# Performance work log

Hardware: AMD Instinct MI355X
Metric: run time of the kernel (lower is better)

Reference implementation:

```python
import jax, jax.numpy as jnp
import numpy as np

EPS_NORM = 1e-8
EPS_Q = 1e-5

def rmsnorm(x, g):
    var = jnp.mean(x * x, axis=-1, keepdims=True)
    return x * jax.lax.rsqrt(var + EPS_NORM) * g

def activation_quant(x):
    # per-token int8 absmax quantization
    scale = 127.0 / jnp.clip(jnp.max(jnp.abs(x), axis=-1, keepdims=True), EPS_Q, None)
    return jnp.clip(jnp.round(x * scale), -128.0, 127.0) / scale

def weight_quant(w):
    # per-tensor ternary absmean quantization
    scale = 1.0 / jnp.clip(jnp.mean(jnp.abs(w)), EPS_Q, None)
    return jnp.clip(jnp.round(w * scale), -1.0, 1.0) / scale

def ste(x, qfn):
    # straight-through estimator: forward quantized, backward identity
    return x + jax.lax.stop_gradient(qfn(x) - x)

def bitlinear(x, w, g):
    h = rmsnorm(x, g)
    hq = ste(h, activation_quant)
    wq = ste(w, weight_quant)
    return jnp.einsum('bsh,oh->bso', hq, wq)

def setup_inputs() -> dict:
    key = jax.random.key(0)
    k1, k2, k3 = jax.random.split(key, 3)
    B, S, H = 2, 2048, 2048
    I = int(H * 4.0)  # intermediate_size = 8192
    x = jax.random.normal(k1, (B, S, H), dtype=jnp.float32)
    w_gate = jax.random.normal(k2, (2 * I, H), dtype=jnp.float32) * 0.02
    g_gate = jnp.ones((H,), dtype=jnp.float32)
    w_down = jax.random.normal(k3, (H, I), dtype=jnp.float32) * 0.02
    g_down = jnp.ones((I,), dtype=jnp.float32)
    return {"x": x, "w_gate": w_gate, "g_gate": g_gate, "w_down": w_down, "g_down": g_down}

def reference(x, w_gate, g_gate, w_down, g_down):
    y = bitlinear(x, w_gate, g_gate)        # [B,S,2I]
    gate, up = jnp.split(y, 2, axis=-1)     # each [B,S,I]
    z = bitlinear(jax.nn.silu(gate) * up, w_down, g_down)  # [B,S,H]
    return z
```

## Files before the change

kernel.cpp:

```cpp
#include <hip/hip_runtime.h>
#include <hip/hip_bf16.h>
#include <hip/hip_fp16.h>

#define DEVINL __device__ __forceinline__

typedef float f32x4 __attribute__((ext_vector_type(4)));
typedef int i32x4 __attribute__((ext_vector_type(4)));
typedef unsigned int u32x4 __attribute__((ext_vector_type(4)));
typedef unsigned int u32x2 __attribute__((ext_vector_type(2)));

typedef __attribute__((address_space(1))) void void_g;
typedef __attribute__((address_space(3))) void void_l;

DEVINL void gload16(const void* g, void* l) {
  __builtin_amdgcn_global_load_lds((void_g*)g, (void_l*)l, 16, 0, 0);
}

DEVINL float wave_sum(float v) {
  #pragma unroll
  for (int o = 32; o > 0; o >>= 1) v += __shfl_down(v, o, 64);
  return v;
}
DEVINL float wave_max(float v) {
  #pragma unroll
  for (int o = 32; o > 0; o >>= 1) v = fmaxf(v, __shfl_down(v, o, 64));
  return v;
}

DEVINL unsigned int pack4(float a, float b, float c, float d) {
  return ((unsigned int)(unsigned char)(signed char)(int)a)
       | (((unsigned int)(unsigned char)(signed char)(int)b) << 8)
       | (((unsigned int)(unsigned char)(signed char)(int)c) << 16)
       | (((unsigned int)(unsigned char)(signed char)(int)d) << 24);
}

__global__ __launch_bounds__(256) void absum_kernel(const float* __restrict__ w,
                                                    long long nchunk, double* __restrict__ out) {
  long long stride = (long long)gridDim.x * 256;
  long long i = (long long)blockIdx.x * 256 + threadIdx.x;
  float s = 0.f;
  for (; i < nchunk; i += stride) {
    f32x4 v = ((const f32x4*)w)[i];
    s += fabsf(v[0]) + fabsf(v[1]) + fabsf(v[2]) + fabsf(v[3]);
  }
  s = wave_sum(s);
  __shared__ float red[4];
  int lane = threadIdx.x & 63, wv = threadIdx.x >> 6;
  if (lane == 0) red[wv] = s;
  __syncthreads();
  if (threadIdx.x == 0) atomicAdd(out, (double)(red[0] + red[1] + red[2] + red[3]));
}

__global__ __launch_bounds__(256) void quantw_kernel(const float* __restrict__ w,
                                                     signed char* __restrict__ tern,
                                                     long long nchunk,
                                                     const double* __restrict__ sum, double inv_n) {
  float scale = (float)(1.0 / fmax(*sum * inv_n, 1e-5));
  long long stride = (long long)gridDim.x * 256;
  long long i = (long long)blockIdx.x * 256 + threadIdx.x;
  for (; i < nchunk; i += stride) {
    f32x4 v0 = ((const f32x4*)w)[2 * i];
    f32x4 v1 = ((const f32x4*)w)[2 * i + 1];
    float t[8];
    #pragma unroll
    for (int k = 0; k < 4; k++) {
      t[k]     = fminf(fmaxf(rintf(v0[k] * scale), -1.f), 1.f);
      t[4 + k] = fminf(fmaxf(rintf(v1[k] * scale), -1.f), 1.f);
    }
    u32x2 o;
    o[0] = pack4(t[0], t[1], t[2], t[3]);
    o[1] = pack4(t[4], t[5], t[6], t[7]);
    ((u32x2*)tern)[i] = o;
  }
}

__global__ __launch_bounds__(256) void actq1_kernel(const float* __restrict__ x,
                                                    const float* __restrict__ g,
                                                    signed char* __restrict__ q,
                                                    float* __restrict__ a) {
  int t = blockIdx.x, tid = threadIdx.x;
  int lane = tid & 63, wv = tid >> 6;
  __shared__ float redS[4], redM[4];

  const f32x4* xr = (const f32x4*)(x + (size_t)t * 2048);
  f32x4 v0 = xr[tid * 2], v1 = xr[tid * 2 + 1];
  float ssq = 0.f;
  #pragma unroll
  for (int k = 0; k < 4; k++) ssq += v0[k] * v0[k] + v1[k] * v1[k];
  float ws_ = wave_sum(ssq);
  if (lane == 0) redS[wv] = ws_;
  __syncthreads();
  float tot = redS[0] + redS[1] + redS[2] + redS[3];
  float r = rsqrtf(tot / 2048.f + 1e-8f);

  f32x4 g0 = ((const f32x4*)g)[tid * 2], g1 = ((const f32x4*)g)[tid * 2 + 1];
  float h[8], amax = 0.f;
  #pragma unroll
  for (int k = 0; k < 4; k++) {
    h[k]     = v0[k] * r * g0[k];
    h[4 + k] = v1[k] * r * g1[k];
    amax = fmaxf(amax, fmaxf(fabsf(h[k]), fabsf(h[4 + k])));
  }
  float wm = wave_max(amax);
  if (lane == 0) redM[wv] = wm;
  __syncthreads();
  float am = fmaxf(fmaxf(fmaxf(redM[0], redM[1]), fmaxf(redM[2], redM[3])), 1e-5f);
  float scale = 127.f / am;

  float qv[8];
  #pragma unroll
  for (int k = 0; k < 8; k++) qv[k] = fminf(fmaxf(rintf(h[k] * scale), -128.f), 127.f);
  u32x2 o;
  o[0] = pack4(qv[0], qv[1], qv[2], qv[3]);
  o[1] = pack4(qv[4], qv[5], qv[6], qv[7]);
  ((u32x2*)(q + (size_t)t * 2048))[tid] = o;
  if (tid == 0) a[t] = am / 127.f;
}

__global__ __launch_bounds__(256) void silu_rms_q_kernel(const unsigned short* __restrict__ y,
                                                         const float* __restrict__ g,
                                                         signed char* __restrict__ q2,
                                                         float* __restrict__ a2) {
  int t = blockIdx.x, tid = threadIdx.x;
  int lane = tid & 63, wv = tid >> 6;
  __shared__ float redS[4], redM[4];
  const u32x4* gate = (const u32x4*)(y + (size_t)t * 16384);
  const u32x4* up   = (const u32x4*)(y + (size_t)t * 16384 + 8192);

  float v[32];
  float ssq = 0.f;
  #pragma unroll
  for (int b = 0; b < 4; b++) {
    u32x4 gr = gate[b * 256 + tid];
    u32x4 ur = up[b * 256 + tid];
    #pragma unroll
    for (int k = 0; k < 4; k++) {
      float g0 = __half2float(__ushort_as_half((unsigned short)(gr[k] & 0xFFFFu)));
      float g1 = __half2float(__ushort_as_half((unsigned short)(gr[k] >> 16)));
      float u0 = __half2float(__ushort_as_half((unsigned short)(ur[k] & 0xFFFFu)));
      float u1 = __half2float(__ushort_as_half((unsigned short)(ur[k] >> 16)));
      float v0 = g0 / (1.f + expf(-g0)) * u0;
      float v1 = g1 / (1.f + expf(-g1)) * u1;
      v[b * 8 + 2 * k] = v0;
      v[b * 8 + 2 * k + 1] = v1;
      ssq += v0 * v0 + v1 * v1;
    }
  }
  float ws_ = wave_sum(ssq);
  if (lane == 0) redS[wv] = ws_;
  __syncthreads();
  float tot = redS[0] + redS[1] + redS[2] + redS[3];
  float r = rsqrtf(tot / 8192.f + 1e-8f);

  float amax = 0.f;
  #pragma unroll
  for (int b = 0; b < 4; b++) {
    f32x4 ga = ((const f32x4*)g)[b * 512 + tid * 2];
    f32x4 gb = ((const f32x4*)g)[b * 512 + tid * 2 + 1];
    #pragma unroll
    for (int k = 0; k < 4; k++) {
      float h0 = v[b * 8 + k]     * r * ga[k];
      float h1 = v[b * 8 + 4 + k] * r * gb[k];
      v[b * 8 + k] = h0;
      v[b * 8 + 4 + k] = h1;
      amax = fmaxf(amax, fmaxf(fabsf(h0), fabsf(h1)));
    }
  }
  float wm = wave_max(amax);
  if (lane == 0) redM[wv] = wm;
  __syncthreads();
  float am = fmaxf(fmaxf(fmaxf(redM[0], redM[1]), fmaxf(redM[2], redM[3])), 1e-5f);
  float scale = 127.f / am;

  #pragma unroll
  for (int b = 0; b < 4; b++) {
    float qv[8];
    #pragma unroll
    for (int k = 0; k < 8; k++)
      qv[k] = fminf(fmaxf(rintf(v[b * 8 + k] * scale), -128.f), 127.f);
    u32x2 o;
    o[0] = pack4(qv[0], qv[1], qv[2], qv[3]);
    o[1] = pack4(qv[4], qv[5], qv[6], qv[7]);
    ((u32x2*)(q2 + (size_t)t * 8192))[b * 256 + tid] = o;
  }
  if (tid == 0) a2[t] = am / 127.f;
}


#define RD16(P, off) (*(const i32x4*)((P) + (off)))
#define MFMA_I8(a, b, c) __builtin_amdgcn_mfma_i32_16x16x64_i8((a), (b), (c), 0, 0, 0)
#define VM0 asm volatile("s_waitcnt vmcnt(0)" ::: "memory");

#define CB(ks) ((((ks) << 6) | sq) ^ sfx)
#define RDA(d0_, d1_, d2_, d3_, h, ks) { const int o_ = arow0 + (h) * 8192 + CB(ks); \
  d0_ = RD16(Ac, o_); d1_ = RD16(Ac, o_ + 2048); d2_ = RD16(Ac, o_ + 4096); d3_ = RD16(Ac, o_ + 6144); }
#define RDB(d0_, d1_, d2_, d3_, ks) { const int o_ = brow0 + CB(ks); \
  d0_ = RD16(Bc, o_); d1_ = RD16(Bc, o_ + 2048); d2_ = RD16(Bc, o_ + 4096); d3_ = RD16(Bc, o_ + 6144); }

#define CL(h, A0_, A1_, A2_, A3_, B0_, B1_, B2_, B3_) \
  __builtin_amdgcn_s_setprio(1); \
  acc[(h)*4+0][0] = MFMA_I8(A0_, B0_, acc[(h)*4+0][0]); \
  acc[(h)*4+0][1] = MFMA_I8(A0_, B1_, acc[(h)*4+0][1]); \
  acc[(h)*4+0][2] = MFMA_I8(A0_, B2_, acc[(h)*4+0][2]); \
  acc[(h)*4+0][3] = MFMA_I8(A0_, B3_, acc[(h)*4+0][3]); \
  acc[(h)*4+1][0] = MFMA_I8(A1_, B0_, acc[(h)*4+1][0]); \
  acc[(h)*4+1][1] = MFMA_I8(A1_, B1_, acc[(h)*4+1][1]); \
  acc[(h)*4+1][2] = MFMA_I8(A1_, B2_, acc[(h)*4+1][2]); \
  acc[(h)*4+1][3] = MFMA_I8(A1_, B3_, acc[(h)*4+1][3]); \
  acc[(h)*4+2][0] = MFMA_I8(A2_, B0_, acc[(h)*4+2][0]); \
  acc[(h)*4+2][1] = MFMA_I8(A2_, B1_, acc[(h)*4+2][1]); \
  acc[(h)*4+2][2] = MFMA_I8(A2_, B2_, acc[(h)*4+2][2]); \
  acc[(h)*4+2][3] = MFMA_I8(A2_, B3_, acc[(h)*4+2][3]); \
  acc[(h)*4+3][0] = MFMA_I8(A3_, B0_, acc[(h)*4+3][0]); \
  acc[(h)*4+3][1] = MFMA_I8(A3_, B1_, acc[(h)*4+3][1]); \
  acc[(h)*4+3][2] = MFMA_I8(A3_, B2_, acc[(h)*4+3][2]); \
  acc[(h)*4+3][3] = MFMA_I8(A3_, B3_, acc[(h)*4+3][3]); \
  __builtin_amdgcn_s_setprio(0);

#define TILE_BODY(S, KA, KB) { \
  i32x4 a0, a1, a2, a3, b0, b1, b2, b3, c0, c1, c2, c3, d0, d1, d2, d3; \
  S \
  RDA(a0, a1, a2, a3, 0, KA)              \
  RDB(b0, b1, b2, b3, KA)                 \
  RDA(c0, c1, c2, c3, 1, KA)              \
  CL(0, a0, a1, a2, a3, b0, b1, b2, b3) \
  RDA(d0, d1, d2, d3, 0, KB)              \
  RDB(a0, a1, a2, a3, KB)                 \
  CL(1, c0, c1, c2, c3, b0, b1, b2, b3) \
  RDA(b0, b1, b2, b3, 1, KB)              \
  CL(0, d0, d1, d2, d3, a0, a1, a2, a3) \
  CL(1, b0, b1, b2, b3, a0, a1, a2, a3) \
}

template <int OUT_MODE>
__global__ __launch_bounds__(512, 2) void gemm256_i8_kernel(
    const signed char* __restrict__ A, const signed char* __restrict__ B,
    void* __restrict__ Cv, int M, int N, int K,
    const float* __restrict__ rowscale, const double* __restrict__ wsum, double inv_n) {
  __shared__ __align__(16) signed char lds[131072];
  const int tid = threadIdx.x;
  const int lane = tid & 63;
  const int wid = tid >> 6;
  const int wr = wid >> 2;
  const int wc = wid & 3;

  const int nbn = N >> 8;
  const int b = blockIdx.x;
  const int cpx = gridDim.x >> 3;
  const int sb = (b & 7) * cpx + (b >> 3);
  const int m0 = (sb / nbn) << 8;
  const int n0 = (sb % nbn) << 8;

  const int fr = lane & 15;
  const int sq = (lane >> 4) << 4;
  const int sfx = (fr & 7) << 4;
  const int arow0 = (wr * 128 + fr) * 128;
  const int brow0 = (wc * 64 + fr) * 128;

  const int rr = tid >> 3;
  const int co = (((tid & 7) ^ (rr & 7)) << 4);
  const signed char* gA = A + (size_t)(m0 + rr) * K + co;
  const signed char* gB = B + (size_t)(n0 + rr) * K + co;
  const size_t g64 = (size_t)64 * K;

  i32x4 acc[8][4] = {};
  const int NT = K >> 7;

  {
    signed char* Ad = lds + tid * 16;
    signed char* Bd = Ad + 32768;
    gload16(gB,           Bd);
    gload16(gB + g64,     Bd + 8192);
    gload16(gB + 2 * g64, Bd + 16384);
    gload16(gB + 3 * g64, Bd + 24576);
    gload16(gA,           Ad);
    gload16(gA + g64,     Ad + 8192);
    gload16(gA + 2 * g64, Ad + 16384);
    gload16(gA + 3 * g64, Ad + 24576);
    VM0
    __builtin_amdgcn_s_barrier();
  }

#define STAGE_ALL \
    gload16(gBt, Bd); gload16(gBt + g64, Bd + 8192); \
    gload16(gBt + 2 * g64, Bd + 16384); gload16(gBt + 3 * g64, Bd + 24576); \
    gload16(gAt, Ad); gload16(gAt + g64, Ad + 8192); \
    gload16(gAt + 2 * g64, Ad + 16384); gload16(gAt + 3 * g64, Ad + 24576);

  for (int t = 0; t < NT - 1; ++t) {
    const signed char* Ac = lds + ((t & 1) << 16);
    const signed char* Bc = Ac + 32768;
    signed char* Ad = lds + (((t & 1) ^ 1) << 16) + tid * 16;
    signed char* Bd = Ad + 32768;
    const signed char* gAt = gA + (size_t)(t + 1) * 128;
    const signed char* gBt = gB + (size_t)(t + 1) * 128;

    if (wid & 1) { TILE_BODY(STAGE_ALL, 1, 0) }
    else         { TILE_BODY(STAGE_ALL, 0, 1) }

    VM0
    __builtin_amdgcn_s_barrier();
  }

  {
    const signed char* Ac = lds + (((NT - 1) & 1) << 16);
    const signed char* Bc = Ac + 32768;
    if (wid & 1) { TILE_BODY(, 1, 0) }
    else         { TILE_BODY(, 0, 1) }
  }

  float sw = (float)fmax(*wsum * inv_n, 1e-5);
  const int qo = lane >> 4;
  const int cb = n0 + wc * 64 + fr;
  #pragma unroll
  for (int ai = 0; ai < 8; ai++) {
    const int rowb = m0 + wr * 128 + ai * 16 + qo * 4;
    #pragma unroll
    for (int r = 0; r < 4; r++) {
      float sc = rowscale[rowb + r] * sw;
      size_t off = (size_t)(rowb + r) * N + cb;
      #pragma unroll
      for (int n = 0; n < 4; n++) {
        float vv = (float)acc[ai][n][r] * sc;
        if (OUT_MODE == 0) ((unsigned short*)Cv)[off + n * 16] = __half_as_ushort(__float2half(vv));
        else               ((float*)Cv)[off + n * 16] = vv;
      }
    }
  }
}

#define CL16(AA0, AA1, AA2, AA3, B0_, B1_, B2_, B3_) \
  __builtin_amdgcn_s_setprio(1); \
  acc[0][0] = MFMA_I8(AA0, B0_, acc[0][0]); \
  acc[0][1] = MFMA_I8(AA0, B1_, acc[0][1]); \
  acc[0][2] = MFMA_I8(AA0, B2_, acc[0][2]); \
  acc[0][3] = MFMA_I8(AA0, B3_, acc[0][3]); \
  acc[1][0] = MFMA_I8(AA1, B0_, acc[1][0]); \
  acc[1][1] = MFMA_I8(AA1, B1_, acc[1][1]); \
  acc[1][2] = MFMA_I8(AA1, B2_, acc[1][2]); \
  acc[1][3] = MFMA_I8(AA1, B3_, acc[1][3]); \
  acc[2][0] = MFMA_I8(AA2, B0_, acc[2][0]); \
  acc[2][1] = MFMA_I8(AA2, B1_, acc[2][1]); \
  acc[2][2] = MFMA_I8(AA2, B2_, acc[2][2]); \
  acc[2][3] = MFMA_I8(AA2, B3_, acc[2][3]); \
  acc[3][0] = MFMA_I8(AA3, B0_, acc[3][0]); \
  acc[3][1] = MFMA_I8(AA3, B1_, acc[3][1]); \
  acc[3][2] = MFMA_I8(AA3, B2_, acc[3][2]); \
  acc[3][3] = MFMA_I8(AA3, B3_, acc[3][3]); \
  __builtin_amdgcn_s_setprio(0);

#define RDA2(d0_, d1_, d2_, d3_, ks) { const int o_ = arow0 + CB(ks); \
  d0_ = RD16(Ac, o_); d1_ = RD16(Ac, o_ + 2048); d2_ = RD16(Ac, o_ + 4096); d3_ = RD16(Ac, o_ + 6144); }

#define TILE_BODY2(S, KA, KB) { \
  i32x4 a0, a1, a2, a3, b0, b1, b2, b3, c0, c1, c2, c3, d0, d1, d2, d3; \
  S \
  RDA2(a0, a1, a2, a3, KA)  RDB(b0, b1, b2, b3, KA) \
  RDA2(c0, c1, c2, c3, KB) \
  CL16(a0, a1, a2, a3, b0, b1, b2, b3) \
  RDB(d0, d1, d2, d3, KB) \
  CL16(c0, c1, c2, c3, d0, d1, d2, d3) \
}

template <int OUT_MODE>
__global__ __launch_bounds__(512, 1) void gemm128_i8_kernel(
    const signed char* __restrict__ A, const signed char* __restrict__ B,
    void* __restrict__ Cv, int M, int N, int K,
    const float* __restrict__ rowscale, const double* __restrict__ wsum, double inv_n) {
  __shared__ __align__(16) signed char lds[98304];
  const int tid = threadIdx.x;
  const int lane = tid & 63;
  const int wid = tid >> 6;
  const int wr = wid >> 2;
  const int wc = wid & 3;

  const int nbn = N >> 8;
  const int b = blockIdx.x;
  const int cpx = gridDim.x >> 3;
  const int sb = (b & 7) * cpx + (b >> 3);
  const int m0 = (sb / nbn) << 7;
  const int n0 = (sb % nbn) << 8;

  const int fr = lane & 15;
  const int sq = (lane >> 4) << 4;
  const int sfx = (fr & 7) << 4;
  const int arow0 = (wr * 64 + fr) * 128;
  const int brow0 = (wc * 64 + fr) * 128;

  const int rr = tid >> 3;
  const int co = (((tid & 7) ^ (rr & 7)) << 4);
  const signed char* gA = A + (size_t)(m0 + rr) * K + co;
  const signed char* gB = B + (size_t)(n0 + rr) * K + co;
  const size_t g64 = (size_t)64 * K;

  i32x4 acc[4][4] = {};
  const int NT = K >> 7;

  {
    signed char* Ad = lds + tid * 16;
    signed char* Bd = Ad + 16384;
    gload16(gB,           Bd);
    gload16(gB + g64,     Bd + 8192);
    gload16(gB + 2 * g64, Bd + 16384);
    gload16(gB + 3 * g64, Bd + 24576);
    gload16(gA,           Ad);
    gload16(gA + g64,     Ad + 8192);
    VM0
    __builtin_amdgcn_s_barrier();
  }

#define STAGE_ALL2 \
    gload16(gBt, Bd); gload16(gBt + g64, Bd + 8192); \
    gload16(gBt + 2 * g64, Bd + 16384); gload16(gBt + 3 * g64, Bd + 24576); \
    gload16(gAt, Ad); gload16(gAt + g64, Ad + 8192);

  for (int t = 0; t < NT - 1; ++t) {
    const signed char* Ac = lds + (t & 1) * 49152;
    const signed char* Bc = Ac + 16384;
    signed char* Ad = lds + ((t & 1) ^ 1) * 49152 + tid * 16;
    signed char* Bd = Ad + 16384;
    const signed char* gAt = gA + (size_t)(t + 1) * 128;
    const signed char* gBt = gB + (size_t)(t + 1) * 128;

    if (wid & 1) { TILE_BODY2(STAGE_ALL2, 1, 0) }
    else         { TILE_BODY2(STAGE_ALL2, 0, 1) }

    VM0
    __builtin_amdgcn_s_barrier();
  }

  {
    const signed char* Ac = lds + ((NT - 1) & 1) * 49152;
    const signed char* Bc = Ac + 16384;
    if (wid & 1) { TILE_BODY2(, 1, 0) }
    else         { TILE_BODY2(, 0, 1) }
  }

  float sw = (float)fmax(*wsum * inv_n, 1e-5);
  const int qo = lane >> 4;
  const int cb = n0 + wc * 64 + fr;
  #pragma unroll
  for (int ai = 0; ai < 4; ai++) {
    const int rowb = m0 + wr * 64 + ai * 16 + qo * 4;
    #pragma unroll
    for (int r = 0; r < 4; r++) {
      float sc = rowscale[rowb + r] * sw;
      size_t off = (size_t)(rowb + r) * N + cb;
      #pragma unroll
      for (int n = 0; n < 4; n++) {
        float vv = (float)acc[ai][n][r] * sc;
        if (OUT_MODE == 0) ((unsigned short*)Cv)[off + n * 16] = __half_as_ushort(__float2half(vv));
        else               ((float*)Cv)[off + n * 16] = vv;
      }
    }
  }
}

extern "C" void kernel_launch(void* const* d_in, const int* in_sizes, int n_in,
                              void* d_out, int out_size, void* d_ws, size_t ws_size,
                              hipStream_t stream) {
  const float* x      = (const float*)d_in[0];
  const float* w_gate = (const float*)d_in[1];
  const float* g_gate = (const float*)d_in[2];
  const float* w_down = (const float*)d_in[3];
  const float* g_down = (const float*)d_in[4];
  float* out = (float*)d_out;

  char* ws = (char*)d_ws;
  double* sums = (double*)ws;
  float* a1 = (float*)(ws + 4096);
  float* a2 = (float*)(ws + 20480);
  const size_t MB = 1024 * 1024;
  signed char* tern_g = (signed char*)(ws + 65536);
  signed char* q2     = tern_g;
  signed char* tern_d = (signed char*)(ws + 65536 + 32 * MB);
  signed char* q1     = (signed char*)(ws + 65536 + 48 * MB);
  unsigned short* yh  = (unsigned short*)(ws + 65536 + 56 * MB);

  hipMemsetAsync(sums, 0, 16, stream);
  absum_kernel<<<2048, 256, 0, stream>>>(w_gate, 33554432LL / 4, sums + 0);
  absum_kernel<<<1024, 256, 0, stream>>>(w_down, 16777216LL / 4, sums + 1);
  quantw_kernel<<<4096, 256, 0, stream>>>(w_gate, tern_g, 33554432LL / 8, sums + 0, 1.0 / 33554432.0);
  quantw_kernel<<<2048, 256, 0, stream>>>(w_down, tern_d, 16777216LL / 8, sums + 1, 1.0 / 16777216.0);
  actq1_kernel<<<4096, 256, 0, stream>>>(x, g_gate, q1, a1);
  gemm256_i8_kernel<0><<<1024, 512, 0, stream>>>(q1, tern_g, yh, 4096, 16384, 2048,
                                                 a1, sums + 0, 1.0 / 33554432.0);
  silu_rms_q_kernel<<<4096, 256, 0, stream>>>(yh, g_down, q2, a2);
  gemm128_i8_kernel<1><<<256, 512, 0, stream>>>(q2, tern_d, out, 4096, 2048, 8192,
                                                a2, sums + 1, 1.0 / 16777216.0);
}
```

Baseline: 591.8 us.

## Switch down-projection GEMM to 128x128 tiles with 4 waves and 512 blocks

```diff
diff --git a/kernel.cpp b/kernel.cpp
--- a/kernel.cpp
+++ b/kernel.cpp
@@ -217,17 +217,17 @@
   acc[(h)*4+3][3] = MFMA_I8(A3_, B3_, acc[(h)*4+3][3]); \
   __builtin_amdgcn_s_setprio(0);
 
-#define TILE_BODY(S, KA, KB) { \
+#define TILE_BODY(S) { \
   i32x4 a0, a1, a2, a3, b0, b1, b2, b3, c0, c1, c2, c3, d0, d1, d2, d3; \
   S \
-  RDA(a0, a1, a2, a3, 0, KA)              \
-  RDB(b0, b1, b2, b3, KA)                 \
-  RDA(c0, c1, c2, c3, 1, KA)              \
+  RDA(a0, a1, a2, a3, 0, 0) \
+  RDB(b0, b1, b2, b3, 0) \
+  RDA(c0, c1, c2, c3, 1, 0) \
   CL(0, a0, a1, a2, a3, b0, b1, b2, b3) \
-  RDA(d0, d1, d2, d3, 0, KB)              \
-  RDB(a0, a1, a2, a3, KB)                 \
+  RDA(d0, d1, d2, d3, 0, 1) \
+  RDB(a0, a1, a2, a3, 1) \
   CL(1, c0, c1, c2, c3, b0, b1, b2, b3) \
-  RDA(b0, b1, b2, b3, 1, KB)              \
+  RDA(b0, b1, b2, b3, 1, 1) \
   CL(0, d0, d1, d2, d3, a0, a1, a2, a3) \
   CL(1, b0, b1, b2, b3, a0, a1, a2, a3) \
 }
@@ -295,8 +295,7 @@
     const signed char* gAt = gA + (size_t)(t + 1) * 128;
     const signed char* gBt = gB + (size_t)(t + 1) * 128;
 
-    if (wid & 1) { TILE_BODY(STAGE_ALL, 1, 0) }
-    else         { TILE_BODY(STAGE_ALL, 0, 1) }
+    TILE_BODY(STAGE_ALL)
 
     VM0
     __builtin_amdgcn_s_barrier();
@@ -305,8 +304,7 @@
   {
     const signed char* Ac = lds + (((NT - 1) & 1) << 16);
     const signed char* Bc = Ac + 32768;
-    if (wid & 1) { TILE_BODY(, 1, 0) }
-    else         { TILE_BODY(, 0, 1) }
+    TILE_BODY()
   }
 
   float sw = (float)fmax(*wsum * inv_n, 1e-5);
@@ -352,34 +350,34 @@
 #define RDA2(d0_, d1_, d2_, d3_, ks) { const int o_ = arow0 + CB(ks); \
   d0_ = RD16(Ac, o_); d1_ = RD16(Ac, o_ + 2048); d2_ = RD16(Ac, o_ + 4096); d3_ = RD16(Ac, o_ + 6144); }
 
-#define TILE_BODY2(S, KA, KB) { \
+#define TILE_BODY2(S) { \
   i32x4 a0, a1, a2, a3, b0, b1, b2, b3, c0, c1, c2, c3, d0, d1, d2, d3; \
   S \
-  RDA2(a0, a1, a2, a3, KA)  RDB(b0, b1, b2, b3, KA) \
-  RDA2(c0, c1, c2, c3, KB) \
+  RDA2(a0, a1, a2, a3, 0)  RDB(b0, b1, b2, b3, 0) \
+  RDA2(c0, c1, c2, c3, 1) \
   CL16(a0, a1, a2, a3, b0, b1, b2, b3) \
-  RDB(d0, d1, d2, d3, KB) \
+  RDB(d0, d1, d2, d3, 1) \
   CL16(c0, c1, c2, c3, d0, d1, d2, d3) \
 }
 
 template <int OUT_MODE>
-__global__ __launch_bounds__(512, 1) void gemm128_i8_kernel(
+__global__ __launch_bounds__(256, 2) void gemm128sq_i8_kernel(
     const signed char* __restrict__ A, const signed char* __restrict__ B,
     void* __restrict__ Cv, int M, int N, int K,
     const float* __restrict__ rowscale, const double* __restrict__ wsum, double inv_n) {
-  __shared__ __align__(16) signed char lds[98304];
+  __shared__ __align__(16) signed char lds[65536];
   const int tid = threadIdx.x;
   const int lane = tid & 63;
   const int wid = tid >> 6;
-  const int wr = wid >> 2;
-  const int wc = wid & 3;
-
-  const int nbn = N >> 8;
+  const int wr = wid >> 1;
+  const int wc = wid & 1;
+
+  const int nbn = N >> 7;
   const int b = blockIdx.x;
   const int cpx = gridDim.x >> 3;
   const int sb = (b & 7) * cpx + (b >> 3);
   const int m0 = (sb / nbn) << 7;
-  const int n0 = (sb % nbn) << 8;
+  const int n0 = (sb % nbn) << 7;
 
   const int fr = lane & 15;
   const int sq = (lane >> 4) << 4;
@@ -391,7 +389,7 @@
   const int co = (((tid & 7) ^ (rr & 7)) << 4);
   const signed char* gA = A + (size_t)(m0 + rr) * K + co;
   const signed char* gB = B + (size_t)(n0 + rr) * K + co;
-  const size_t g64 = (size_t)64 * K;
+  const size_t g32 = (size_t)32 * K;
 
   i32x4 acc[4][4] = {};
   const int NT = K >> 7;
@@ -400,40 +398,41 @@
     signed char* Ad = lds + tid * 16;
     signed char* Bd = Ad + 16384;
     gload16(gB,           Bd);
-    gload16(gB + g64,     Bd + 8192);
-    gload16(gB + 2 * g64, Bd + 16384);
-    gload16(gB + 3 * g64, Bd + 24576);
+    gload16(gB + g32,     Bd + 4096);
+    gload16(gB + 2 * g32, Bd + 8192);
+    gload16(gB + 3 * g32, Bd + 12288);
     gload16(gA,           Ad);
-    gload16(gA + g64,     Ad + 8192);
+    gload16(gA + g32,     Ad + 4096);
+    gload16(gA + 2 * g32, Ad + 8192);
+    gload16(gA + 3 * g32, Ad + 12288);
     VM0
     __builtin_amdgcn_s_barrier();
   }
 
 #define STAGE_ALL2 \
-    gload16(gBt, Bd); gload16(gBt + g64, Bd + 8192); \
-    gload16(gBt + 2 * g64, Bd + 16384); gload16(gBt + 3 * g64, Bd + 24576); \
-    gload16(gAt, Ad); gload16(gAt + g64, Ad + 8192);
+    gload16(gBt, Bd); gload16(gBt + g32, Bd + 4096); \
+    gload16(gBt + 2 * g32, Bd + 8192); gload16(gBt + 3 * g32, Bd + 12288); \
+    gload16(gAt, Ad); gload16(gAt + g32, Ad + 4096); \
+    gload16(gAt + 2 * g32, Ad + 8192); gload16(gAt + 3 * g32, Ad + 12288);
 
   for (int t = 0; t < NT - 1; ++t) {
-    const signed char* Ac = lds + (t & 1) * 49152;
+    const signed char* Ac = lds + ((t & 1) << 15);
     const signed char* Bc = Ac + 16384;
-    signed char* Ad = lds + ((t & 1) ^ 1) * 49152 + tid * 16;
+    signed char* Ad = lds + (((t & 1) ^ 1) << 15) + tid * 16;
     signed char* Bd = Ad + 16384;
     const signed char* gAt = gA + (size_t)(t + 1) * 128;
     const signed char* gBt = gB + (size_t)(t + 1) * 128;
 
-    if (wid & 1) { TILE_BODY2(STAGE_ALL2, 1, 0) }
-    else         { TILE_BODY2(STAGE_ALL2, 0, 1) }
+    TILE_BODY2(STAGE_ALL2)
 
     VM0
     __builtin_amdgcn_s_barrier();
   }
 
   {
-    const signed char* Ac = lds + ((NT - 1) & 1) * 49152;
+    const signed char* Ac = lds + (((NT - 1) & 1) << 15);
     const signed char* Bc = Ac + 16384;
-    if (wid & 1) { TILE_BODY2(, 1, 0) }
-    else         { TILE_BODY2(, 0, 1) }
+    TILE_BODY2()
   }
 
   float sw = (float)fmax(*wsum * inv_n, 1e-5);
@@ -486,6 +485,6 @@
   gemm256_i8_kernel<0><<<1024, 512, 0, stream>>>(q1, tern_g, yh, 4096, 16384, 2048,
                                                  a1, sums + 0, 1.0 / 33554432.0);
   silu_rms_q_kernel<<<4096, 256, 0, stream>>>(yh, g_down, q2, a2);
-  gemm128_i8_kernel<1><<<256, 512, 0, stream>>>(q2, tern_d, out, 4096, 2048, 8192,
-                                                a2, sums + 1, 1.0 / 16777216.0);
-}
+  gemm128sq_i8_kernel<1><<<512, 256, 0, stream>>>(q2, tern_d, out, 4096, 2048, 8192,
+                                                  a2, sums + 1, 1.0 / 16777216.0);
+}
```

After: 562.3 us. 1.05x faster.
